# Optimization experiments

Measured on AMD Instinct MI355X. Metric: run time of the kernel, lower is better.

## Reference

```python
import jax, jax.numpy as jnp
import numpy as np
import math

B, S, D = 1, 2048, 2048
NH, NKV = 32, 8
HD = D // NH  # 64
N_REP = NH // NKV


def _rope_tables(seq_len, head_dim, base=10000.0):
    half = head_dim // 2
    inv_freq = 1.0 / (base ** (np.arange(half, dtype=np.float32) / half))
    ang = np.arange(seq_len, dtype=np.float32)[:, None] * inv_freq[None, :]  # [S, half]
    ang = np.concatenate([ang, ang], axis=-1)  # [S, head_dim]
    cos = jnp.asarray(np.cos(ang))[:, None, :]  # [S, 1, head_dim]
    sin = jnp.asarray(np.sin(ang))[:, None, :]
    return cos, sin


def setup_inputs() -> dict:
    key = jax.random.key(0)
    ks = jax.random.split(key, 5)
    x = jax.random.normal(ks[0], (B, S, D), dtype=jnp.float32)
    cos, sin = _rope_tables(S, HD)
    # causal additive mask, broadcast over batch/heads
    neg = jnp.float32(-1e9)
    causal = jnp.where(jnp.tril(jnp.ones((S, S), dtype=bool)), 0.0, neg)
    mask = causal[None, None, :, :]  # [1,1,S,S]
    scale = 0.02
    wq = jax.random.normal(ks[1], (D, NH * HD), dtype=jnp.float32) * scale
    wk = jax.random.normal(ks[2], (D, NKV * HD), dtype=jnp.float32) * scale
    wv = jax.random.normal(ks[3], (D, NKV * HD), dtype=jnp.float32) * scale
    wo = jax.random.normal(ks[4], (NH * HD, D), dtype=jnp.float32) * scale
    return {"x": x, "cos": cos, "sin": sin, "mask": mask,
            "wq": wq, "wk": wk, "wv": wv, "wo": wo}


def apply_rotary_emb(x, cos, sin):
    # x: [b, s, h, d]; cos/sin: [s, 1, d] (broadcast over b, h)
    half = x.shape[-1] // 2
    x1, x2 = x[..., :half], x[..., half:]
    c, s = cos[..., :half], sin[..., :half]
    return jnp.concatenate([x1 * c - x2 * s, x1 * s + x2 * c], axis=-1)


def reference(x, cos, sin, mask, wq, wk, wv, wo):
    b, s, _ = x.shape
    q = (x @ wq).reshape(b, s, NH, HD)
    k = (x @ wk).reshape(b, s, NKV, HD)
    v = (x @ wv).reshape(b, s, NKV, HD)
    q = apply_rotary_emb(q, cos, sin)
    k = apply_rotary_emb(k, cos, sin)
    new_k, new_v = k, v  # kv cache (no previous cache)
    # GQA: repeat_interleave kv heads to match query heads
    k_rep = jnp.repeat(k, N_REP, axis=2)  # [b, s, NH, HD]
    v_rep = jnp.repeat(v, N_REP, axis=2)
    scores = jnp.einsum('bqhd,bkhd->bhqk', q, k_rep) / math.sqrt(HD)
    scores = scores + mask[:, :, -s:, :]
    attn = jax.nn.softmax(scores.astype(jnp.float32), axis=-1).astype(q.dtype)
    out = jnp.einsum('bhqk,bkhd->bqhd', attn, v_rep).reshape(b, s, NH * HD)
    return out @ wo, new_k, new_v
```

## Files before the change

kernel.cpp:

```cpp
#include <hip/hip_runtime.h>

#define S_LEN 2048
#define NHQ 32
#define NKV 8
#define HD 64
#define DMODEL 2048
#define DKV 512

typedef unsigned short ushort_t;
typedef unsigned int uint_t;

typedef __attribute__((ext_vector_type(8))) short bf16x8;
typedef __attribute__((ext_vector_type(4))) float f32x4;

__device__ __forceinline__ float b2f(ushort_t h) {
  union { uint_t u; float f; } v;
  v.u = ((uint_t)h) << 16;
  return v.f;
}
__device__ __forceinline__ ushort_t f2b(float f) {
  union { float f; uint_t u; } v;
  v.f = f;
  uint_t r = v.u + 0x7fffu + ((v.u >> 16) & 1u);
  return (ushort_t)(r >> 16);
}
__device__ __forceinline__ uint_t pack2(float lo, float hi) {
  return (uint_t)f2b(lo) | ((uint_t)f2b(hi) << 16);
}

union BF8 { uint4 v; ushort_t s[8]; };

__device__ __forceinline__ void gl_lds16(const ushort_t* g, ushort_t* l) {
  __builtin_amdgcn_global_load_lds((const __attribute__((address_space(1))) void*)g,
                                   (__attribute__((address_space(3))) void*)l, 16, 0, 0);
}

__global__ void xb_kernel(const float* __restrict__ X, ushort_t* __restrict__ XB) {
  int i = (blockIdx.x * 256 + threadIdx.x) * 8;
  float4 a = *(const float4*)(X + i);
  float4 b = *(const float4*)(X + i + 4);
  BF8 u;
  u.s[0] = f2b(a.x); u.s[1] = f2b(a.y); u.s[2] = f2b(a.z); u.s[3] = f2b(a.w);
  u.s[4] = f2b(b.x); u.s[5] = f2b(b.y); u.s[6] = f2b(b.z); u.s[7] = f2b(b.w);
  *(uint4*)(XB + i) = u.v;
}

__global__ __launch_bounds__(256) void wT_kernel(const float* __restrict__ W,
                                                 ushort_t* __restrict__ WT,
                                                 int K, int N) {
  __shared__ ushort_t T[64][66];
  const int tid = threadIdx.x;
  const int r0 = blockIdx.x * 64;
  const int c0 = blockIdx.y * 64;
  {
    const int rl = tid >> 2, cp = (tid & 3) * 16;
    const float* p = W + (size_t)(r0 + rl) * N + c0 + cp;
    float v[16];
    *(float4*)(v)      = *(const float4*)(p);
    *(float4*)(v + 4)  = *(const float4*)(p + 4);
    *(float4*)(v + 8)  = *(const float4*)(p + 8);
    *(float4*)(v + 12) = *(const float4*)(p + 12);
    #pragma unroll
    for (int j = 0; j < 16; ++j) T[cp + j][rl] = f2b(v[j]);
  }
  __syncthreads();
  {
    const int cl = tid >> 2, rp = (tid & 3) * 16;
    uint_t u[8];
    #pragma unroll
    for (int i = 0; i < 8; ++i) u[i] = *(const uint_t*)&T[cl][rp + 2 * i];
    ushort_t* outp = WT + (size_t)(c0 + cl) * K + r0 + rp;
    *(uint4*)(outp)     = make_uint4(u[0], u[1], u[2], u[3]);
    *(uint4*)(outp + 8) = make_uint4(u[4], u[5], u[6], u[7]);
  }
}

__device__ __forceinline__ void gemm_core_gl(const ushort_t* __restrict__ A,
                                             const ushort_t* __restrict__ BT,
                                             int K, int tile_m, int tile_n,
                                             f32x4 (&acc)[4][2],
                                             ushort_t (*As)[32], ushort_t (*Bs)[32]) {
  const int tid = threadIdx.x;
  const int lane = tid & 63;
  const int w = tid >> 6;
  const int wr = (w >> 1) * 64, wc = (w & 1) * 32;
  const int lm = lane & 15, kq = lane >> 4;

  #pragma unroll
  for (int i = 0; i < 4; ++i)
    #pragma unroll
    for (int j = 0; j < 2; ++j) acc[i][j] = {0.f, 0.f, 0.f, 0.f};

  const ushort_t* ap0 = A  + (size_t)(tile_m + w * 32 + (lane >> 2)) * K + (lane & 3) * 8;
  const ushort_t* ap1 = ap0 + (size_t)16 * K;
  const ushort_t* bp  = BT + (size_t)(tile_n + w * 16 + (lane >> 2)) * K + (lane & 3) * 8;
  ushort_t* asb0 = &As[0][0] + w * 1024;
  ushort_t* asb1 = asb0 + 512;
  ushort_t* bsb  = &Bs[0][0] + w * 512;

  for (int kt = 0; kt < K; kt += 32) {
    __syncthreads();
    gl_lds16(ap0 + kt, asb0);
    gl_lds16(ap1 + kt, asb1);
    gl_lds16(bp  + kt, bsb);
    __syncthreads();
    bf16x8 af[4], bfr[2];
    #pragma unroll
    for (int i = 0; i < 4; ++i) af[i]  = *(const bf16x8*)&As[wr + 16 * i + lm][kq * 8];
    #pragma unroll
    for (int j = 0; j < 2; ++j) bfr[j] = *(const bf16x8*)&Bs[wc + 16 * j + lm][kq * 8];
    #pragma unroll
    for (int i = 0; i < 4; ++i)
      #pragma unroll
      for (int j = 0; j < 2; ++j)
        acc[i][j] = __builtin_amdgcn_mfma_f32_16x16x32_bf16(af[i], bfr[j], acc[i][j], 0, 0, 0);
  }
}

__global__ __launch_bounds__(256) void gemm_proj(const ushort_t* __restrict__ A,
                                                 const ushort_t* __restrict__ BT,
                                                 ushort_t* __restrict__ Qo,
                                                 float* __restrict__ Ko,
                                                 float* __restrict__ Vo) {
  __shared__ ushort_t As[128][32];
  __shared__ ushort_t Bs[64][32];
  const int lane = threadIdx.x & 63;
  const int w = threadIdx.x >> 6;
  const int wr = (w >> 1) * 64, wc = (w & 1) * 32;
  const int lm = lane & 15, kq = lane >> 4;
  const int tile_m = blockIdx.y * 128, tile_n = blockIdx.x * 64;
  f32x4 acc[4][2];
  gemm_core_gl(A, BT, DMODEL, tile_m, tile_n, acc, As, Bs);
  #pragma unroll
  for (int i = 0; i < 4; ++i)
    #pragma unroll
    for (int j = 0; j < 2; ++j)
      #pragma unroll
      for (int r = 0; r < 4; ++r) {
        const int row = tile_m + wr + 16 * i + kq * 4 + r;
        const int col = tile_n + wc + 16 * j + lm;
        const float v = acc[i][j][r];
        if (col < 2048)      Qo[(size_t)row * DMODEL + col] = f2b(v);
        else if (col < 2560) Ko[(size_t)row * DKV + col - 2048] = v;
        else                 Vo[(size_t)row * DKV + col - 2560] = v;
      }
}

__global__ __launch_bounds__(256) void gemm_out(const ushort_t* __restrict__ A,
                                                const ushort_t* __restrict__ BT,
                                                float* __restrict__ C) {
  __shared__ ushort_t As[128][32];
  __shared__ ushort_t Bs[64][32];
  const int lane = threadIdx.x & 63;
  const int w = threadIdx.x >> 6;
  const int wr = (w >> 1) * 64, wc = (w & 1) * 32;
  const int lm = lane & 15, kq = lane >> 4;
  const int tile_m = blockIdx.y * 128, tile_n = blockIdx.x * 64;
  f32x4 acc[4][2];
  gemm_core_gl(A, BT, DMODEL, tile_m, tile_n, acc, As, Bs);
  #pragma unroll
  for (int i = 0; i < 4; ++i)
    #pragma unroll
    for (int j = 0; j < 2; ++j)
      #pragma unroll
      for (int r = 0; r < 4; ++r) {
        const int row = tile_m + wr + 16 * i + kq * 4 + r;
        const int col = tile_n + wc + 16 * j + lm;
        C[(size_t)row * DMODEL + col] = acc[i][j][r];
      }
}

__global__ void rope_kb_kernel(float* Kio, ushort_t* __restrict__ KB,
                               const float* __restrict__ cosT, const float* __restrict__ sinT) {
  int idx = blockIdx.x * 256 + threadIdx.x;
  int d = idx & 31;
  int hk = (idx >> 5) & 7;
  int s = idx >> 8;
  float* p = Kio + (size_t)s * DKV + hk * HD + d;
  float x1 = p[0], x2 = p[32];
  float c = cosT[s * 64 + d], sn = sinT[s * 64 + d];
  float n1 = x1 * c - x2 * sn;
  float n2 = x1 * sn + x2 * c;
  p[0] = n1; p[32] = n2;
  ushort_t* kb = KB + (size_t)hk * S_LEN * HD + (size_t)s * HD + d;
  kb[0] = f2b(n1); kb[32] = f2b(n2);
}

__global__ __launch_bounds__(256) void vt_kernel(const float* __restrict__ V,
                                                 ushort_t* __restrict__ VT) {
  __shared__ ushort_t T[64][66];
  const int tid = threadIdx.x;
  const int s0 = blockIdx.x * 64;
  const int hk = blockIdx.y;
  {
    const int s_l = tid >> 2, dp = (tid & 3) * 16;
    const float* p = V + (size_t)(s0 + s_l) * DKV + hk * HD + dp;
    float v[16];
    *(float4*)(v)      = *(const float4*)(p);
    *(float4*)(v + 4)  = *(const float4*)(p + 4);
    *(float4*)(v + 8)  = *(const float4*)(p + 8);
    *(float4*)(v + 12) = *(const float4*)(p + 12);
    #pragma unroll
    for (int j = 0; j < 16; ++j) T[dp + j][s_l] = f2b(v[j]);
  }
  __syncthreads();
  {
    const int d_l = tid >> 2, sp = (tid & 3) * 16;
    uint_t u[8];
    #pragma unroll
    for (int i = 0; i < 8; ++i) u[i] = *(const uint_t*)&T[d_l][sp + 2 * i];
    ushort_t* outp = VT + (size_t)hk * HD * S_LEN + (size_t)d_l * S_LEN + s0 + sp;
    *(uint4*)(outp)     = make_uint4(u[0], u[1], u[2], u[3]);
    *(uint4*)(outp + 8) = make_uint4(u[4], u[5], u[6], u[7]);
  }
}

__global__ __launch_bounds__(128) void attn_mfma2(const ushort_t* Q,
                                                  const ushort_t* __restrict__ KB,
                                                  const ushort_t* __restrict__ VT,
                                                  const float* __restrict__ cosT,
                                                  const float* __restrict__ sinT,
                                                  ushort_t* O) {
  __shared__ ushort_t Ps[2][32][66];
  const int wv = threadIdx.x >> 6;
  const int lane = threadIdx.x & 63;
  const int lm = lane & 15, kq = lane >> 4;
  const int h = blockIdx.x >> 5;
  const int pr_ = blockIdx.x & 31;
  const int g = wv ? (63 - pr_) : pr_;
  const int q0 = g * 32;
  const int hk = h >> 2;
  const ushort_t* KBh = KB + (size_t)hk * S_LEN * HD;
  const ushort_t* VTh = VT + (size_t)hk * HD * S_LEN;
  const float SCL = 0.125f * 1.44269504f;

  bf16x8 bq[2][2];
  #pragma unroll
  for (int nt = 0; nt < 2; ++nt) {
    const int row = q0 + 16 * nt + lm;
    const ushort_t* qp = Q + (size_t)row * DMODEL + h * HD + 8 * kq;
    bf16x8 x1v = *(const bf16x8*)qp;
    bf16x8 x2v = *(const bf16x8*)(qp + 32);
    const float* cp = cosT + row * 64 + 8 * kq;
    const float* sp = sinT + row * 64 + 8 * kq;
    float c[8], s[8];
    *(float4*)(c)     = *(const float4*)(cp);
    *(float4*)(c + 4) = *(const float4*)(cp + 4);
    *(float4*)(s)     = *(const float4*)(sp);
    *(float4*)(s + 4) = *(const float4*)(sp + 4);
    BF8 o1, o2;
    #pragma unroll
    for (int j = 0; j < 8; ++j) {
      float x1 = b2f((ushort_t)x1v[j]);
      float x2 = b2f((ushort_t)x2v[j]);
      o1.s[j] = f2b(x1 * c[j] - x2 * s[j]);
      o2.s[j] = f2b(x1 * s[j] + x2 * c[j]);
    }
    bq[nt][0] = *(const bf16x8*)&o1;
    bq[nt][1] = *(const bf16x8*)&o2;
  }

  f32x4 Oa[4][2];
  #pragma unroll
  for (int mt = 0; mt < 4; ++mt) { Oa[mt][0] = {0.f,0.f,0.f,0.f}; Oa[mt][1] = {0.f,0.f,0.f,0.f}; }
  float m[2] = {-1e30f, -1e30f}, l[2] = {0.f, 0.f};

  const int ntiles = (q0 + 31) / 64 + 1;
  for (int t = 0; t < ntiles; ++t) {
    const int base = t * 64;
    f32x4 sc[4][2];
    #pragma unroll
    for (int mt = 0; mt < 4; ++mt) { sc[mt][0] = {0.f,0.f,0.f,0.f}; sc[mt][1] = {0.f,0.f,0.f,0.f}; }
    #pragma unroll
    for (int kc = 0; kc < 2; ++kc) {
      bf16x8 ak[4];
      #pragma unroll
      for (int mt = 0; mt < 4; ++mt)
        ak[mt] = *(const bf16x8*)&KBh[(size_t)(base + 16 * mt + lm) * HD + 8 * kq + 32 * kc];
      #pragma unroll
      for (int mt = 0; mt < 4; ++mt)
        #pragma unroll
        for (int nt = 0; nt < 2; ++nt)
          sc[mt][nt] = __builtin_amdgcn_mfma_f32_16x16x32_bf16(ak[mt], bq[nt][kc], sc[mt][nt], 0, 0, 0);
    }
    const bool diag = (t == ntiles - 1);
    #pragma unroll
    for (int nt = 0; nt < 2; ++nt) {
      const int qg = q0 + 16 * nt + lm;
      #pragma unroll
      for (int mt = 0; mt < 4; ++mt)
        #pragma unroll
        for (int r = 0; r < 4; ++r) {
          float sv = sc[mt][nt][r] * SCL;
          if (diag && (base + 16 * mt + 4 * kq + r > qg)) sv = -1e9f;
          sc[mt][nt][r] = sv;
        }
      float mx = sc[0][nt][0];
      #pragma unroll
      for (int mt = 0; mt < 4; ++mt)
        #pragma unroll
        for (int r = 0; r < 4; ++r) mx = fmaxf(mx, sc[mt][nt][r]);
      mx = fmaxf(mx, __shfl_xor(mx, 16));
      mx = fmaxf(mx, __shfl_xor(mx, 32));
      const float mn = fmaxf(m[nt], mx);
      const float al = exp2f(m[nt] - mn);
      m[nt] = mn;
      float sum = 0.f;
      #pragma unroll
      for (int mt = 0; mt < 4; ++mt)
        #pragma unroll
        for (int r = 0; r < 4; ++r) {
          float p = exp2f(sc[mt][nt][r] - mn);
          sc[mt][nt][r] = p;
          sum += p;
        }
      sum += __shfl_xor(sum, 16);
      sum += __shfl_xor(sum, 32);
      l[nt] = l[nt] * al + sum;
      #pragma unroll
      for (int mt = 0; mt < 4; ++mt)
        #pragma unroll
        for (int r = 0; r < 4; ++r) Oa[mt][nt][r] *= al;
      ushort_t* pw = &Ps[wv][16 * nt + lm][4 * kq];
      #pragma unroll
      for (int mt = 0; mt < 4; ++mt) {
        *(uint_t*)(pw + 16 * mt)     = pack2(sc[mt][nt][0], sc[mt][nt][1]);
        *(uint_t*)(pw + 16 * mt + 2) = pack2(sc[mt][nt][2], sc[mt][nt][3]);
      }
    }
    #pragma unroll
    for (int kc = 0; kc < 2; ++kc) {
      bf16x8 av[4], pb[2];
      #pragma unroll
      for (int mt = 0; mt < 4; ++mt)
        av[mt] = *(const bf16x8*)&VTh[(size_t)(16 * mt + lm) * S_LEN + base + 8 * kq + 32 * kc];
      #pragma unroll
      for (int nt = 0; nt < 2; ++nt) {
        const ushort_t* prr = &Ps[wv][16 * nt + lm][8 * kq + 32 * kc];
        union { uint_t u[4]; bf16x8 v; } pu;
        pu.u[0] = *(const uint_t*)(prr);
        pu.u[1] = *(const uint_t*)(prr + 2);
        pu.u[2] = *(const uint_t*)(prr + 4);
        pu.u[3] = *(const uint_t*)(prr + 6);
        pb[nt] = pu.v;
      }
      #pragma unroll
      for (int mt = 0; mt < 4; ++mt)
        #pragma unroll
        for (int nt = 0; nt < 2; ++nt)
          Oa[mt][nt] = __builtin_amdgcn_mfma_f32_16x16x32_bf16(av[mt], pb[nt], Oa[mt][nt], 0, 0, 0);
    }
  }
  #pragma unroll
  for (int nt = 0; nt < 2; ++nt) {
    const float inv = 1.f / l[nt];
    ushort_t* orow = O + (size_t)(q0 + 16 * nt + lm) * DMODEL + h * HD + 4 * kq;
    #pragma unroll
    for (int mt = 0; mt < 4; ++mt) {
      *(uint_t*)(orow + 16 * mt)     = pack2(Oa[mt][nt][0] * inv, Oa[mt][nt][1] * inv);
      *(uint_t*)(orow + 16 * mt + 2) = pack2(Oa[mt][nt][2] * inv, Oa[mt][nt][3] * inv);
    }
  }
}

extern "C" void kernel_launch(void* const* d_in, const int* in_sizes, int n_in,
                              void* d_out, int out_size, void* d_ws, size_t ws_size,
                              hipStream_t stream) {
  const float* x    = (const float*)d_in[0];
  const float* cosT = (const float*)d_in[1];
  const float* sinT = (const float*)d_in[2];
  const float* wq   = (const float*)d_in[4];
  const float* wk   = (const float*)d_in[5];
  const float* wv   = (const float*)d_in[6];
  const float* wo   = (const float*)d_in[7];

  float* out   = (float*)d_out;
  float* out_k = out + (size_t)S_LEN * DMODEL;
  float* out_v = out_k + (size_t)S_LEN * DKV;

  const size_t MB = 1024 * 1024;
  ushort_t* ws    = (ushort_t*)d_ws;
  ushort_t* wqT   = ws;
  ushort_t* wkT   = ws + 4 * MB;
  ushort_t* ws_q  = ws + 6 * MB;
  ushort_t* ws_kb = ws + 10 * MB;
  ushort_t* ws_vt = ws + 11 * MB;
  ushort_t* xb    = (ushort_t*)out;

  dim3 blk(256);
  xb_kernel<<<(S_LEN * DMODEL / 8) / 256, 256, 0, stream>>>(x, xb);
  wT_kernel<<<dim3(32, 32), blk, 0, stream>>>(wq, wqT, DMODEL, DMODEL);
  wT_kernel<<<dim3(32, 8),  blk, 0, stream>>>(wk, wkT, DMODEL, DKV);
  wT_kernel<<<dim3(32, 8),  blk, 0, stream>>>(wv, wkT + (size_t)DKV * DMODEL, DMODEL, DKV);
  gemm_proj<<<dim3(3072 / 64, S_LEN / 128), blk, 0, stream>>>(xb, wqT, ws_q, out_k, out_v);
  wT_kernel<<<dim3(32, 32), blk, 0, stream>>>(wo, wqT, DMODEL, DMODEL);
  rope_kb_kernel<<<(S_LEN * NKV * 32) / 256, 256, 0, stream>>>(out_k, ws_kb, cosT, sinT);
  vt_kernel<<<dim3(S_LEN / 64, NKV), blk, 0, stream>>>(out_v, ws_vt);
  attn_mfma2<<<NHQ * 32, 128, 0, stream>>>(ws_q, ws_kb, ws_vt, cosT, sinT, ws_q);
  gemm_out<<<dim3(DMODEL / 64, S_LEN / 128), blk, 0, stream>>>(ws_q, wqT, out);
}
```

Measured before the change: 305.5 us.

## Split attention KV range across wave pairs with lazy rescale and merge

The attention kernel now runs four waves per block. Each query tile is handled by two waves that take alternating KV tiles, and their partial outputs, maxima and sums are combined through shared memory at the end. It also folds the softmax scale into Q during RoPE, skips rescaling the accumulator unless the running max grows by more than 8 in log2 units, uses the hardware packed bf16 convert, and raises wave priority around MFMA blocks. This doubles the parallelism per query tile and trims VALU work, at the cost of a shared-memory merge step and a slight precision change from rounding Q after scaling.

```diff
diff --git a/kernel.cpp b/kernel.cpp
--- a/kernel.cpp
+++ b/kernel.cpp
@@ -26,6 +26,11 @@
 }
 __device__ __forceinline__ uint_t pack2(float lo, float hi) {
   return (uint_t)f2b(lo) | ((uint_t)f2b(hi) << 16);
+}
+__device__ __forceinline__ uint_t cvt_pk_bf16(float lo, float hi) {
+  uint_t r;
+  asm("v_cvt_pk_bf16_f32 %0, %1, %2" : "=v"(r) : "v"(lo), "v"(hi));
+  return r;
 }
 
 union BF8 { uint4 v; ushort_t s[8]; };
@@ -215,19 +220,21 @@
   }
 }
 
-__global__ __launch_bounds__(128) void attn_mfma2(const ushort_t* Q,
+__global__ __launch_bounds__(256) void attn_mfma3(const ushort_t* Q,
                                                   const ushort_t* __restrict__ KB,
                                                   const ushort_t* __restrict__ VT,
                                                   const float* __restrict__ cosT,
                                                   const float* __restrict__ sinT,
                                                   ushort_t* O) {
-  __shared__ ushort_t Ps[2][32][66];
+  __shared__ __align__(16) char smem[20480];
+  ushort_t (*Ps)[32][66] = (ushort_t (*)[32][66])smem;
   const int wv = threadIdx.x >> 6;
   const int lane = threadIdx.x & 63;
   const int lm = lane & 15, kq = lane >> 4;
   const int h = blockIdx.x >> 5;
   const int pr_ = blockIdx.x & 31;
-  const int g = wv ? (63 - pr_) : pr_;
+  const int g = (wv & 2) ? (63 - pr_) : pr_;
+  const int half = wv & 1;
   const int q0 = g * 32;
   const int hk = h >> 2;
   const ushort_t* KBh = KB + (size_t)hk * S_LEN * HD;
@@ -253,8 +260,8 @@
     for (int j = 0; j < 8; ++j) {
       float x1 = b2f((ushort_t)x1v[j]);
       float x2 = b2f((ushort_t)x2v[j]);
-      o1.s[j] = f2b(x1 * c[j] - x2 * s[j]);
-      o2.s[j] = f2b(x1 * s[j] + x2 * c[j]);
+      o1.s[j] = f2b((x1 * c[j] - x2 * s[j]) * SCL);
+      o2.s[j] = f2b((x1 * s[j] + x2 * c[j]) * SCL);
     }
     bq[nt][0] = *(const bf16x8*)&o1;
     bq[nt][1] = *(const bf16x8*)&o2;
@@ -266,7 +273,7 @@
   float m[2] = {-1e30f, -1e30f}, l[2] = {0.f, 0.f};
 
   const int ntiles = (q0 + 31) / 64 + 1;
-  for (int t = 0; t < ntiles; ++t) {
+  for (int t = half; t < ntiles; t += 2) {
     const int base = t * 64;
     f32x4 sc[4][2];
     #pragma unroll
@@ -277,24 +284,25 @@
       #pragma unroll
       for (int mt = 0; mt < 4; ++mt)
         ak[mt] = *(const bf16x8*)&KBh[(size_t)(base + 16 * mt + lm) * HD + 8 * kq + 32 * kc];
+      __builtin_amdgcn_s_setprio(1);
       #pragma unroll
       for (int mt = 0; mt < 4; ++mt)
         #pragma unroll
         for (int nt = 0; nt < 2; ++nt)
           sc[mt][nt] = __builtin_amdgcn_mfma_f32_16x16x32_bf16(ak[mt], bq[nt][kc], sc[mt][nt], 0, 0, 0);
+      __builtin_amdgcn_s_setprio(0);
     }
     const bool diag = (t == ntiles - 1);
     #pragma unroll
     for (int nt = 0; nt < 2; ++nt) {
       const int qg = q0 + 16 * nt + lm;
-      #pragma unroll
-      for (int mt = 0; mt < 4; ++mt)
-        #pragma unroll
-        for (int r = 0; r < 4; ++r) {
-          float sv = sc[mt][nt][r] * SCL;
-          if (diag && (base + 16 * mt + 4 * kq + r > qg)) sv = -1e9f;
-          sc[mt][nt][r] = sv;
-        }
+      if (diag) {
+        #pragma unroll
+        for (int mt = 0; mt < 4; ++mt)
+          #pragma unroll
+          for (int r = 0; r < 4; ++r)
+            if (base + 16 * mt + 4 * kq + r > qg) sc[mt][nt][r] = -1e9f;
+      }
       float mx = sc[0][nt][0];
       #pragma unroll
       for (int mt = 0; mt < 4; ++mt)
@@ -302,30 +310,33 @@
         for (int r = 0; r < 4; ++r) mx = fmaxf(mx, sc[mt][nt][r]);
       mx = fmaxf(mx, __shfl_xor(mx, 16));
       mx = fmaxf(mx, __shfl_xor(mx, 32));
-      const float mn = fmaxf(m[nt], mx);
-      const float al = exp2f(m[nt] - mn);
-      m[nt] = mn;
+      if (!__all(mx <= m[nt] + 8.f)) {
+        const float mn = fmaxf(m[nt], mx);
+        const float al = exp2f(m[nt] - mn);
+        m[nt] = mn;
+        l[nt] *= al;
+        #pragma unroll
+        for (int mt = 0; mt < 4; ++mt)
+          #pragma unroll
+          for (int r = 0; r < 4; ++r) Oa[mt][nt][r] *= al;
+      }
       float sum = 0.f;
       #pragma unroll
       for (int mt = 0; mt < 4; ++mt)
         #pragma unroll
         for (int r = 0; r < 4; ++r) {
-          float p = exp2f(sc[mt][nt][r] - mn);
+          float p = exp2f(sc[mt][nt][r] - m[nt]);
           sc[mt][nt][r] = p;
           sum += p;
         }
       sum += __shfl_xor(sum, 16);
       sum += __shfl_xor(sum, 32);
-      l[nt] = l[nt] * al + sum;
-      #pragma unroll
-      for (int mt = 0; mt < 4; ++mt)
-        #pragma unroll
-        for (int r = 0; r < 4; ++r) Oa[mt][nt][r] *= al;
+      l[nt] += sum;
       ushort_t* pw = &Ps[wv][16 * nt + lm][4 * kq];
       #pragma unroll
       for (int mt = 0; mt < 4; ++mt) {
-        *(uint_t*)(pw + 16 * mt)     = pack2(sc[mt][nt][0], sc[mt][nt][1]);
-        *(uint_t*)(pw + 16 * mt + 2) = pack2(sc[mt][nt][2], sc[mt][nt][3]);
+        *(uint_t*)(pw + 16 * mt)     = cvt_pk_bf16(sc[mt][nt][0], sc[mt][nt][1]);
+        *(uint_t*)(pw + 16 * mt + 2) = cvt_pk_bf16(sc[mt][nt][2], sc[mt][nt][3]);
       }
     }
     #pragma unroll
@@ -344,21 +355,56 @@
         pu.u[3] = *(const uint_t*)(prr + 6);
         pb[nt] = pu.v;
       }
+      __builtin_amdgcn_s_setprio(1);
       #pragma unroll
       for (int mt = 0; mt < 4; ++mt)
         #pragma unroll
         for (int nt = 0; nt < 2; ++nt)
           Oa[mt][nt] = __builtin_amdgcn_mfma_f32_16x16x32_bf16(av[mt], pb[nt], Oa[mt][nt], 0, 0, 0);
-    }
-  }
-  #pragma unroll
-  for (int nt = 0; nt < 2; ++nt) {
-    const float inv = 1.f / l[nt];
-    ushort_t* orow = O + (size_t)(q0 + 16 * nt + lm) * DMODEL + h * HD + 4 * kq;
-    #pragma unroll
-    for (int mt = 0; mt < 4; ++mt) {
-      *(uint_t*)(orow + 16 * mt)     = pack2(Oa[mt][nt][0] * inv, Oa[mt][nt][1] * inv);
-      *(uint_t*)(orow + 16 * mt + 2) = pack2(Oa[mt][nt][2] * inv, Oa[mt][nt][3] * inv);
+      __builtin_amdgcn_s_setprio(0);
+    }
+  }
+
+  __syncthreads();
+  float* CoB = (float*)smem;
+  float* CmB = (float*)smem + 2 * 64 * 36;
+  float* ClB = CmB + 2 * 2 * 64;
+  const int pair = wv >> 1;
+  if (half) {
+    float* myo = CoB + (size_t)(pair * 64 + lane) * 36;
+    #pragma unroll
+    for (int mt = 0; mt < 4; ++mt)
+      #pragma unroll
+      for (int nt = 0; nt < 2; ++nt)
+        *(f32x4*)(myo + (mt * 2 + nt) * 4) = Oa[mt][nt];
+    #pragma unroll
+    for (int nt = 0; nt < 2; ++nt) {
+      CmB[(pair * 2 + nt) * 64 + lane] = m[nt];
+      ClB[(pair * 2 + nt) * 64 + lane] = l[nt];
+    }
+  }
+  __syncthreads();
+  if (!half) {
+    const float* po = CoB + (size_t)(pair * 64 + lane) * 36;
+    #pragma unroll
+    for (int nt = 0; nt < 2; ++nt) {
+      const float m1 = CmB[(pair * 2 + nt) * 64 + lane];
+      const float l1 = ClB[(pair * 2 + nt) * 64 + lane];
+      const float mn = fmaxf(m[nt], m1);
+      const float a0 = exp2f(m[nt] - mn);
+      const float a1 = exp2f(m1 - mn);
+      const float inv = 1.f / (l[nt] * a0 + l1 * a1);
+      ushort_t* orow = O + (size_t)(q0 + 16 * nt + lm) * DMODEL + h * HD + 4 * kq;
+      #pragma unroll
+      for (int mt = 0; mt < 4; ++mt) {
+        const f32x4 o1 = *(const f32x4*)(po + (mt * 2 + nt) * 4);
+        const float v0 = (Oa[mt][nt][0] * a0 + o1[0] * a1) * inv;
+        const float v1 = (Oa[mt][nt][1] * a0 + o1[1] * a1) * inv;
+        const float v2 = (Oa[mt][nt][2] * a0 + o1[2] * a1) * inv;
+        const float v3 = (Oa[mt][nt][3] * a0 + o1[3] * a1) * inv;
+        *(uint_t*)(orow + 16 * mt)     = cvt_pk_bf16(v0, v1);
+        *(uint_t*)(orow + 16 * mt + 2) = cvt_pk_bf16(v2, v3);
+      }
     }
   }
 }
@@ -396,6 +442,6 @@
   wT_kernel<<<dim3(32, 32), blk, 0, stream>>>(wo, wqT, DMODEL, DMODEL);
   rope_kb_kernel<<<(S_LEN * NKV * 32) / 256, 256, 0, stream>>>(out_k, ws_kb, cosT, sinT);
   vt_kernel<<<dim3(S_LEN / 64, NKV), blk, 0, stream>>>(out_v, ws_vt);
-  attn_mfma2<<<NHQ * 32, 128, 0, stream>>>(ws_q, ws_kb, ws_vt, cosT, sinT, ws_q);
+  attn_mfma3<<<NHQ * 32, 256, 0, stream>>>(ws_q, ws_kb, ws_vt, cosT, sinT, ws_q);
   gemm_out<<<dim3(DMODEL / 64, S_LEN / 128), blk, 0, stream>>>(ws_q, wqT, out);
 }
```

Measured after the change: 308.5 us. No clear change (+1.0%).
